# Optimization experiments

Measured on AMD Instinct MI355X. Metric: run time of the kernel, lower is better.

Reference implementation:

```python
import jax, jax.numpy as jnp
import numpy as np

H = 128  # hidden size

def lstm_layer(x, Wih, Whh, bih, bhh):
    """One PyTorch-semantics LSTM layer. x: (B,T,F). Gate order: i,f,g,o."""
    B = x.shape[0]
    # Precompute input contributions for all timesteps: (B,T,4H)
    xg = jnp.einsum('btf,gf->btg', x, Wih) + bih + bhh
    def step(carry, xt):
        h, c = carry
        g = xt + h @ Whh.T                      # (B,4H)
        i, f, gg, o = jnp.split(g, 4, axis=-1)
        i = jax.nn.sigmoid(i)
        f = jax.nn.sigmoid(f)
        gg = jnp.tanh(gg)
        o = jax.nn.sigmoid(o)
        c = f * c + i * gg
        h = o * jnp.tanh(c)
        return (h, c), h
    h0 = jnp.zeros((B, H), x.dtype)
    (hT, cT), hs = jax.lax.scan(step, (h0, h0), jnp.swapaxes(xg, 0, 1))
    return jnp.swapaxes(hs, 0, 1), hT  # (B,T,H), (B,H)


def setup_inputs() -> dict:
    key = jax.random.key(0)
    ks = jax.random.split(key, 20)
    B, T = 256, 2048
    s = 1.0 / np.sqrt(H)  # PyTorch default init scale
    inp = {
        'x': jax.random.normal(ks[0], (B, T, 1), jnp.float32),
        'Wih0': jax.random.uniform(ks[1], (4 * H, 1), jnp.float32, -s, s),
        'Whh0': jax.random.uniform(ks[2], (4 * H, H), jnp.float32, -s, s),
        'bih0': jax.random.uniform(ks[3], (4 * H,), jnp.float32, -s, s),
        'bhh0': jax.random.uniform(ks[4], (4 * H,), jnp.float32, -s, s),
        'Wih1': jax.random.uniform(ks[5], (4 * H, H), jnp.float32, -s, s),
        'Whh1': jax.random.uniform(ks[6], (4 * H, H), jnp.float32, -s, s),
        'bih1': jax.random.uniform(ks[7], (4 * H,), jnp.float32, -s, s),
        'bhh1': jax.random.uniform(ks[8], (4 * H,), jnp.float32, -s, s),
        'Wih2': jax.random.uniform(ks[9], (4 * H, H), jnp.float32, -s, s),
        'Whh2': jax.random.uniform(ks[10], (4 * H, H), jnp.float32, -s, s),
        'bih2': jax.random.uniform(ks[11], (4 * H,), jnp.float32, -s, s),
        'bhh2': jax.random.uniform(ks[12], (4 * H,), jnp.float32, -s, s),
        'fc1_w': jax.random.uniform(ks[13], (64, H), jnp.float32, -s, s),
        'fc1_b': jax.random.uniform(ks[14], (64,), jnp.float32, -s, s),
        'fc2_w': jax.random.uniform(ks[15], (5, 64), jnp.float32, -1.0 / 8, 1.0 / 8),
        'fc2_b': jax.random.uniform(ks[16], (5,), jnp.float32, -1.0 / 8, 1.0 / 8),
    }
    return inp


def reference(x, Wih0, Whh0, bih0, bhh0, Wih1, Whh1, bih1, bhh1,
              Wih2, Whh2, bih2, bhh2, fc1_w, fc1_b, fc2_w, fc2_b):
    # 3-layer LSTM (eval mode: inter-layer dropout is identity)
    h1, _ = lstm_layer(x, Wih0, Whh0, bih0, bhh0)
    h2, _ = lstm_layer(h1, Wih1, Whh1, bih1, bhh1)
    _, hT = lstm_layer(h2, Wih2, Whh2, bih2, bhh2)  # hn[-1]: (B,H)
    z = jax.nn.relu(hT @ fc1_w.T + fc1_b)
    return z @ fc2_w.T + fc2_b  # (B, num_classes)
```

## Files before the change

kernel.cpp:

```cpp
#include <hip/hip_runtime.h>


#define HDIM 128
#define TDIM 2048
#define NB 16
#define NG 16
#define CH 16
#define NCH 128
#define NT 512

typedef _Float16 half8_t __attribute__((ext_vector_type(8)));
typedef float f32x4 __attribute__((ext_vector_type(4)));

__device__ __forceinline__ f32x4 mfma16(half8_t a, half8_t b, f32x4 c) {
    return __builtin_amdgcn_mfma_f32_16x16x32_f16(a, b, c, 0, 0, 0);
}

__device__ __forceinline__ void fast_barrier() {
    asm volatile("s_waitcnt lgkmcnt(0)\n\ts_barrier" ::: "memory");
}

__device__ __forceinline__ float sigm_f(float x) {
    return __builtin_amdgcn_rcpf(1.0f + __expf(-x));
}
__device__ __forceinline__ float tanh_f(float x) {
    return fmaf(-2.0f, __builtin_amdgcn_rcpf(1.0f + __expf(2.0f * x)), 1.0f);
}

__global__ __launch_bounds__(256)
void convert_w(const float* __restrict__ Whh0, const float* __restrict__ Wih1,
               const float* __restrict__ Whh1, const float* __restrict__ Wih2,
               const float* __restrict__ Whh2, _Float16* __restrict__ dst,
               int* __restrict__ flags) {
    int i = blockIdx.x * 256 + threadIdx.x;
    if (i < 2 * NG * NCH) flags[i] = 0;
    int seg = i >> 16, off = i & 65535;
    const float* s = (seg == 0) ? Whh0 : (seg == 1) ? Wih1 : (seg == 2) ? Whh1
                   : (seg == 3) ? Wih2 : Whh2;
    dst[i] = (_Float16)s[off];
}

__global__ __launch_bounds__(NT, 2)
void lstm3_pipe(const float* __restrict__ x,   const float* __restrict__ Wih0,
                const float* __restrict__ bih0, const float* __restrict__ bhh0,
                const float* __restrict__ bih1, const float* __restrict__ bhh1,
                const float* __restrict__ bih2, const float* __restrict__ bhh2,
                const float* __restrict__ fc1w, const float* __restrict__ fc1b,
                const float* __restrict__ fc2w, const float* __restrict__ fc2b,
                float* __restrict__ out,
                _Float16* __restrict__ hbuf, const _Float16* __restrict__ wbuf,
                int* __restrict__ flags)
{
    __shared__ __align__(16) _Float16 hown[CH * NB * HDIM];
    __shared__ __align__(16) _Float16 hst [CH * NB * HDIM];
    __shared__ float x_s[CH][NB];
    __shared__ float z_s[NB][64];
    __shared__ float hfin[NB][HDIM];

    const int tid = threadIdx.x;
    const int ln = tid & 63, wv = tid >> 6;
    const int c = ln & 15, p = ln >> 4;
    const int L = blockIdx.x >> 4;
    const int g = blockIdx.x & 15;

    const _Float16* whh = wbuf + (size_t)((L == 0) ? 0 : (L == 1) ? 2 : 4) * 65536;
    const _Float16* wih = wbuf + (size_t)((L == 1) ? 1 : 3) * 65536;
    half8_t whh_f[4][4], wih_f[4][4];
#pragma unroll
    for (int q = 0; q < 4; ++q)
#pragma unroll
        for (int m = 0; m < 4; ++m) {
            whh_f[q][m] = *(const half8_t*)(whh + (size_t)(q*HDIM + wv*16 + c)*HDIM + m*32 + p*8);
            if (L > 0)
                wih_f[q][m] = *(const half8_t*)(wih + (size_t)(q*HDIM + wv*16 + c)*HDIM + m*32 + p*8);
        }

    const float* bihL = (L == 0) ? bih0 : (L == 1) ? bih1 : bih2;
    const float* bhhL = (L == 0) ? bhh0 : (L == 1) ? bhh1 : bhh2;
    const int u = wv * 16 + c;
    float bias[4], w0[4];
#pragma unroll
    for (int q = 0; q < 4; ++q) {
        bias[q] = bihL[q*HDIM + u] + bhhL[q*HDIM + u];
        w0[q] = (L == 0) ? Wih0[q*HDIM + u] : 0.0f;
    }

    int roff[4], woff[4];
#pragma unroll
    for (int m = 0; m < 4; ++m)
        roff[m] = c*HDIM + ((32*m + 8*p) ^ (8*(c & 7)));
#pragma unroll
    for (int r = 0; r < 4; ++r) {
        int seq = p*4 + r;
        woff[r] = seq*HDIM + (u ^ (8*(seq & 7)));
    }

    for (int i = tid; i < NB*HDIM/2; i += NT)
        ((int*)(hown + 15*NB*HDIM))[i] = 0;
    float cc[4] = {0.f, 0.f, 0.f, 0.f};
    __syncthreads();

    int* fprod = flags + (L*NG + g)*NCH;
    int* fcons = flags + ((L-1)*NG + g)*NCH;
    const float* xb = x + (size_t)(g*NB)*TDIM;

#pragma unroll 1
    for (int s = 0; s < NCH; ++s) {
        _Float16* gch = hbuf + ((size_t)(g*NCH + s) << 15);

        if (L == 0) {
            if (tid < CH*NB)
                x_s[tid >> 4][tid & 15] = xb[(size_t)(tid & 15)*TDIM + s*CH + (tid >> 4)];
        } else {
            if (tid == 0) {
                while (__hip_atomic_load(fcons + s, __ATOMIC_ACQUIRE,
                                         __HIP_MEMORY_SCOPE_AGENT) == 0)
                    __builtin_amdgcn_s_sleep(8);
            }
            __syncthreads();
            const float4* gsrc = (const float4*)gch;
            float4* dv = (float4*)hst;
#pragma unroll
            for (int k2 = 0; k2 < 8; ++k2) dv[k2*NT + tid] = gsrc[k2*NT + tid];
        }
        fast_barrier();

#pragma unroll 1
        for (int tt = 0; tt < CH; ++tt) {
            const int tp = (tt + CH - 1) & 15;
            const _Float16* rsl = hown + tp*(NB*HDIM);
            const _Float16* psl = hst  + tt*(NB*HDIM);
            half8_t A0 = *(const half8_t*)(rsl + roff[0]);
            half8_t A1 = *(const half8_t*)(rsl + roff[1]);
            half8_t A2 = *(const half8_t*)(rsl + roff[2]);
            half8_t A3 = *(const half8_t*)(rsl + roff[3]);

            f32x4 acc[4];
            if (L > 0) {
                half8_t P0 = *(const half8_t*)(psl + roff[0]);
                half8_t P1 = *(const half8_t*)(psl + roff[1]);
                half8_t P2 = *(const half8_t*)(psl + roff[2]);
                half8_t P3 = *(const half8_t*)(psl + roff[3]);
#pragma unroll
                for (int q = 0; q < 4; ++q) {
                    f32x4 a = {0.f, 0.f, 0.f, 0.f};
                    a = mfma16(P0, wih_f[q][0], a);
                    a = mfma16(P1, wih_f[q][1], a);
                    a = mfma16(P2, wih_f[q][2], a);
                    a = mfma16(P3, wih_f[q][3], a);
                    acc[q] = a;
                }
            } else {
#pragma unroll
                for (int q = 0; q < 4; ++q) acc[q] = (f32x4){0.f, 0.f, 0.f, 0.f};
            }
#pragma unroll
            for (int q = 0; q < 4; ++q) {
                acc[q] = mfma16(A0, whh_f[q][0], acc[q]);
                acc[q] = mfma16(A1, whh_f[q][1], acc[q]);
                acc[q] = mfma16(A2, whh_f[q][2], acc[q]);
                acc[q] = mfma16(A3, whh_f[q][3], acc[q]);
            }

            _Float16* wsl = hown + tt*(NB*HDIM);
#pragma unroll
            for (int r = 0; r < 4; ++r) {
                float pi = acc[0][r] + bias[0];
                float pf = acc[1][r] + bias[1];
                float pg = acc[2][r] + bias[2];
                float po = acc[3][r] + bias[3];
                if (L == 0) {
                    float xr = x_s[tt][p*4 + r];
                    pi = fmaf(xr, w0[0], pi); pf = fmaf(xr, w0[1], pf);
                    pg = fmaf(xr, w0[2], pg); po = fmaf(xr, w0[3], po);
                }
                float ig = sigm_f(pi), fg = sigm_f(pf);
                float gg = tanh_f(pg), og = sigm_f(po);
                cc[r] = fmaf(fg, cc[r], ig * gg);
                wsl[woff[r]] = (_Float16)(og * tanh_f(cc[r]));
            }
            fast_barrier();
        }

        if (L < 2) {
            const float4* sv = (const float4*)hown;
            float4* gdst = (float4*)gch;
#pragma unroll
            for (int k2 = 0; k2 < 8; ++k2) gdst[k2*NT + tid] = sv[k2*NT + tid];
            __threadfence();
            __syncthreads();
            if (tid == 0)
                __hip_atomic_store(fprod + s, 1, __ATOMIC_RELEASE,
                                   __HIP_MEMORY_SCOPE_AGENT);
        }
    }

    if (L == 2) {
        __syncthreads();
        for (int i = tid; i < NB*HDIM; i += NT) {
            int seq = i >> 7, uu = i & 127;
            hfin[seq][uu] = (float)hown[15*NB*HDIM + seq*HDIM + (uu ^ (8*(seq & 7)))];
        }
        __syncthreads();
        for (int d = tid; d < NB*64; d += NT) {
            int seq = d >> 6, un = d & 63;
            const float4* w4 = (const float4*)(fc1w + un*HDIM);
            const float4* h4 = (const float4*)hfin[seq];
            float sacc = fc1b[un];
#pragma unroll
            for (int k2 = 0; k2 < 32; ++k2) {
                float4 a = w4[k2], bb = h4[k2];
                sacc += a.x*bb.x + a.y*bb.y + a.z*bb.z + a.w*bb.w;
            }
            z_s[seq][un] = fmaxf(sacc, 0.0f);
        }
        __syncthreads();
        for (int d = tid; d < NB*5; d += NT) {
            int seq = d / 5, o = d - seq*5;
            const float* w = fc2w + o*64;
            float sacc = fc2b[o];
#pragma unroll
            for (int k2 = 0; k2 < 64; ++k2) sacc += w[k2] * z_s[seq][k2];
            out[(size_t)(g*NB + seq)*5 + o] = sacc;
        }
    }
}

extern "C" void kernel_launch(void* const* d_in, const int* in_sizes, int n_in,
                              void* d_out, int out_size, void* d_ws, size_t ws_size,
                              hipStream_t stream) {
    (void)in_sizes; (void)n_in; (void)out_size; (void)ws_size;
    const float* x    = (const float*)d_in[0];
    const float* Wih0 = (const float*)d_in[1];
    const float* Whh0 = (const float*)d_in[2];
    const float* bih0 = (const float*)d_in[3];
    const float* bhh0 = (const float*)d_in[4];
    const float* Wih1 = (const float*)d_in[5];
    const float* Whh1 = (const float*)d_in[6];
    const float* bih1 = (const float*)d_in[7];
    const float* bhh1 = (const float*)d_in[8];
    const float* Wih2 = (const float*)d_in[9];
    const float* Whh2 = (const float*)d_in[10];
    const float* bih2 = (const float*)d_in[11];
    const float* bhh2 = (const float*)d_in[12];
    const float* fc1w = (const float*)d_in[13];
    const float* fc1b = (const float*)d_in[14];
    const float* fc2w = (const float*)d_in[15];
    const float* fc2b = (const float*)d_in[16];
    float* out = (float*)d_out;

    _Float16* hbuf = (_Float16*)d_ws;
    _Float16* wbuf = hbuf + (size_t)67108864;
    int* flags = (int*)(wbuf + (size_t)5*65536);

    hipLaunchKernelGGL(convert_w, dim3(1280), dim3(256), 0, stream,
                       Whh0, Wih1, Whh1, Wih2, Whh2, wbuf, flags);
    hipLaunchKernelGGL(lstm3_pipe, dim3(3*NG), dim3(NT), 0, stream,
                       x, Wih0, bih0, bhh0, bih1, bhh1, bih2, bhh2,
                       fc1w, fc1b, fc2w, fc2b, out, hbuf, wbuf, flags);
}
```

Measured before the change: 3.733 ms.

## Stream input weights from memory, reorder MFMAs, use cache-bypassing inter-layer handoff

The input-to-hidden weight fragments are no longer held in registers. They are reloaded from global memory on every timestep, which lowers register pressure but adds per-step memory traffic. The recurrent h·Whh MFMAs now issue first so the critical dependency starts earlier, and the input projection goes into a separate accumulator. The inter-layer producer/consumer handoff swaps atomics and __threadfence for inline-asm sc0 sc1 loads and stores with a shorter sleep, aiming to cut synchronisation latency. The ordering guarantees of the hand-written flag protocol now rest on those cache bits rather than on acquire/release semantics.

```diff
diff --git a/kernel.cpp b/kernel.cpp
--- a/kernel.cpp
+++ b/kernel.cpp
@@ -65,15 +65,13 @@
 
     const _Float16* whh = wbuf + (size_t)((L == 0) ? 0 : (L == 1) ? 2 : 4) * 65536;
     const _Float16* wih = wbuf + (size_t)((L == 1) ? 1 : 3) * 65536;
-    half8_t whh_f[4][4], wih_f[4][4];
+    half8_t whh_f[4][4];
 #pragma unroll
     for (int q = 0; q < 4; ++q)
 #pragma unroll
-        for (int m = 0; m < 4; ++m) {
+        for (int m = 0; m < 4; ++m)
             whh_f[q][m] = *(const half8_t*)(whh + (size_t)(q*HDIM + wv*16 + c)*HDIM + m*32 + p*8);
-            if (L > 0)
-                wih_f[q][m] = *(const half8_t*)(wih + (size_t)(q*HDIM + wv*16 + c)*HDIM + m*32 + p*8);
-        }
+    const _Float16* wihL = wih + (size_t)(wv*16 + c)*HDIM + p*8;
 
     const float* bihL = (L == 0) ? bih0 : (L == 1) ? bih1 : bih2;
     const float* bhhL = (L == 0) ? bhh0 : (L == 1) ? bhh1 : bhh2;
@@ -101,7 +99,7 @@
     __syncthreads();
 
     int* fprod = flags + (L*NG + g)*NCH;
-    int* fcons = flags + ((L-1)*NG + g)*NCH;
+    const int* fcons = flags + ((L-1)*NG + g)*NCH;
     const float* xb = x + (size_t)(g*NB)*TDIM;
 
 #pragma unroll 1
@@ -113,13 +111,19 @@
                 x_s[tid >> 4][tid & 15] = xb[(size_t)(tid & 15)*TDIM + s*CH + (tid >> 4)];
         } else {
             if (tid == 0) {
-                while (__hip_atomic_load(fcons + s, __ATOMIC_ACQUIRE,
-                                         __HIP_MEMORY_SCOPE_AGENT) == 0)
-                    __builtin_amdgcn_s_sleep(8);
+                const int* fp = fcons + s;
+                int f;
+                while (1) {
+                    asm volatile("global_load_dword %0, %1, off sc0 sc1\n\t"
+                                 "s_waitcnt vmcnt(0)"
+                                 : "=v"(f) : "v"(fp) : "memory");
+                    if (f) break;
+                    __builtin_amdgcn_s_sleep(2);
+                }
             }
             __syncthreads();
-            const float4* gsrc = (const float4*)gch;
-            float4* dv = (float4*)hst;
+            const f32x4* gsrc = (const f32x4*)gch;
+            f32x4* dv = (f32x4*)hst;
 #pragma unroll
             for (int k2 = 0; k2 < 8; ++k2) dv[k2*NT + tid] = gsrc[k2*NT + tid];
         }
@@ -129,37 +133,41 @@
         for (int tt = 0; tt < CH; ++tt) {
             const int tp = (tt + CH - 1) & 15;
             const _Float16* rsl = hown + tp*(NB*HDIM);
-            const _Float16* psl = hst  + tt*(NB*HDIM);
             half8_t A0 = *(const half8_t*)(rsl + roff[0]);
             half8_t A1 = *(const half8_t*)(rsl + roff[1]);
             half8_t A2 = *(const half8_t*)(rsl + roff[2]);
             half8_t A3 = *(const half8_t*)(rsl + roff[3]);
 
-            f32x4 acc[4];
+            f32x4 acc[4], pac[4];
+#pragma unroll
+            for (int q = 0; q < 4; ++q) {
+                f32x4 a = {0.f, 0.f, 0.f, 0.f};
+                a = mfma16(A0, whh_f[q][0], a);
+                a = mfma16(A1, whh_f[q][1], a);
+                a = mfma16(A2, whh_f[q][2], a);
+                a = mfma16(A3, whh_f[q][3], a);
+                acc[q] = a;
+            }
             if (L > 0) {
+                const _Float16* psl = hst + tt*(NB*HDIM);
                 half8_t P0 = *(const half8_t*)(psl + roff[0]);
                 half8_t P1 = *(const half8_t*)(psl + roff[1]);
                 half8_t P2 = *(const half8_t*)(psl + roff[2]);
                 half8_t P3 = *(const half8_t*)(psl + roff[3]);
 #pragma unroll
                 for (int q = 0; q < 4; ++q) {
+                    const _Float16* wq = wihL + q*(HDIM*HDIM);
+                    half8_t B0 = *(const half8_t*)(wq);
+                    half8_t B1 = *(const half8_t*)(wq + 32);
+                    half8_t B2 = *(const half8_t*)(wq + 64);
+                    half8_t B3 = *(const half8_t*)(wq + 96);
                     f32x4 a = {0.f, 0.f, 0.f, 0.f};
-                    a = mfma16(P0, wih_f[q][0], a);
-                    a = mfma16(P1, wih_f[q][1], a);
-                    a = mfma16(P2, wih_f[q][2], a);
-                    a = mfma16(P3, wih_f[q][3], a);
-                    acc[q] = a;
+                    a = mfma16(P0, B0, a);
+                    a = mfma16(P1, B1, a);
+                    a = mfma16(P2, B2, a);
+                    a = mfma16(P3, B3, a);
+                    pac[q] = a;
                 }
-            } else {
-#pragma unroll
-                for (int q = 0; q < 4; ++q) acc[q] = (f32x4){0.f, 0.f, 0.f, 0.f};
-            }
-#pragma unroll
-            for (int q = 0; q < 4; ++q) {
-                acc[q] = mfma16(A0, whh_f[q][0], acc[q]);
-                acc[q] = mfma16(A1, whh_f[q][1], acc[q]);
-                acc[q] = mfma16(A2, whh_f[q][2], acc[q]);
-                acc[q] = mfma16(A3, whh_f[q][3], acc[q]);
             }
 
             _Float16* wsl = hown + tt*(NB*HDIM);
@@ -169,7 +177,10 @@
                 float pf = acc[1][r] + bias[1];
                 float pg = acc[2][r] + bias[2];
                 float po = acc[3][r] + bias[3];
-                if (L == 0) {
+                if (L > 0) {
+                    pi += pac[0][r]; pf += pac[1][r];
+                    pg += pac[2][r]; po += pac[3][r];
+                } else {
                     float xr = x_s[tt][p*4 + r];
                     pi = fmaf(xr, w0[0], pi); pf = fmaf(xr, w0[1], pf);
                     pg = fmaf(xr, w0[2], pg); po = fmaf(xr, w0[3], po);
@@ -183,15 +194,22 @@
         }
 
         if (L < 2) {
-            const float4* sv = (const float4*)hown;
-            float4* gdst = (float4*)gch;
-#pragma unroll
-            for (int k2 = 0; k2 < 8; ++k2) gdst[k2*NT + tid] = sv[k2*NT + tid];
-            __threadfence();
+            const f32x4* sv = (const f32x4*)hown;
+#pragma unroll
+            for (int k2 = 0; k2 < 8; ++k2) {
+                f32x4 v = sv[k2*NT + tid];
+                f32x4* gp = (f32x4*)gch + k2*NT + tid;
+                asm volatile("global_store_dwordx4 %0, %1, off sc0 sc1"
+                             :: "v"(gp), "v"(v) : "memory");
+            }
+            asm volatile("s_waitcnt vmcnt(0)" ::: "memory");
             __syncthreads();
-            if (tid == 0)
-                __hip_atomic_store(fprod + s, 1, __ATOMIC_RELEASE,
-                                   __HIP_MEMORY_SCOPE_AGENT);
+            if (tid == 0) {
+                int one = 1;
+                int* fp = fprod + s;
+                asm volatile("global_store_dword %0, %1, off sc0 sc1"
+                             :: "v"(fp), "v"(one) : "memory");
+            }
         }
     }
 
```

Measured after the change: 9.202 ms. +146.5%, slower.

## Split batch into 64 groups of 4 sequences and prescale gates for exp2

Applied to the files above, without the earlier changes.

Cuts the per-block batch from 16 to 4 sequences and raises the group count from 16 to 64, so 192 blocks run the layer pipeline instead of 48. Each MFMA row-block now holds 4 sequences spaced 4 rows apart, so each lane handles one gate element per step. Weights and biases are prescaled by -log2(e) (doubled for the g gate) so the activations use exp2 directly. Bias is also folded into the accumulator init. The recurrent MFMA work per block stays the same, so this trades a lot of wasted MFMA rows for more parallel chains and less activation math per thread, and it also changes the LDS layout and the global exchange format.

```diff
diff --git a/kernel.cpp b/kernel.cpp
--- a/kernel.cpp
+++ b/kernel.cpp
@@ -3,14 +3,16 @@
 
 #define HDIM 128
 #define TDIM 2048
-#define NB 16
-#define NG 16
+#define NB 4
+#define NG 64
 #define CH 16
 #define NCH 128
 #define NT 512
+#define SLICE 2048
 
 typedef _Float16 half8_t __attribute__((ext_vector_type(8)));
 typedef float f32x4 __attribute__((ext_vector_type(4)));
+typedef int int4v __attribute__((ext_vector_type(4)));
 
 __device__ __forceinline__ f32x4 mfma16(half8_t a, half8_t b, f32x4 c) {
     return __builtin_amdgcn_mfma_f32_16x16x32_f16(a, b, c, 0, 0, 0);
@@ -20,12 +22,11 @@
     asm volatile("s_waitcnt lgkmcnt(0)\n\ts_barrier" ::: "memory");
 }
 
-__device__ __forceinline__ float sigm_f(float x) {
-    return __builtin_amdgcn_rcpf(1.0f + __expf(-x));
-}
-__device__ __forceinline__ float tanh_f(float x) {
-    return fmaf(-2.0f, __builtin_amdgcn_rcpf(1.0f + __expf(2.0f * x)), 1.0f);
-}
+__device__ __forceinline__ float rcpf(float x) { return __builtin_amdgcn_rcpf(x); }
+__device__ __forceinline__ float ex2(float x)  { return __builtin_amdgcn_exp2f(x); }
+
+#define NL2E  -1.4426950408889634f
+#define N2L2E -2.8853900817779268f
 
 __global__ __launch_bounds__(256)
 void convert_w(const float* __restrict__ Whh0, const float* __restrict__ Wih1,
@@ -37,10 +38,12 @@
     int seg = i >> 16, off = i & 65535;
     const float* s = (seg == 0) ? Whh0 : (seg == 1) ? Wih1 : (seg == 2) ? Whh1
                    : (seg == 3) ? Wih2 : Whh2;
-    dst[i] = (_Float16)s[off];
-}
-
-__global__ __launch_bounds__(NT, 2)
+    int gate = off >> 14;
+    float sc = (gate == 2) ? N2L2E : NL2E;
+    dst[i] = (_Float16)(s[off] * sc);
+}
+
+__global__ __launch_bounds__(NT, 1)
 void lstm3_pipe(const float* __restrict__ x,   const float* __restrict__ Wih0,
                 const float* __restrict__ bih0, const float* __restrict__ bhh0,
                 const float* __restrict__ bih1, const float* __restrict__ bhh1,
@@ -51,8 +54,8 @@
                 _Float16* __restrict__ hbuf, const _Float16* __restrict__ wbuf,
                 int* __restrict__ flags)
 {
-    __shared__ __align__(16) _Float16 hown[CH * NB * HDIM];
-    __shared__ __align__(16) _Float16 hst [CH * NB * HDIM];
+    __shared__ __align__(16) _Float16 hown[CH * SLICE];
+    __shared__ __align__(16) _Float16 hst [CH * SLICE];
     __shared__ float x_s[CH][NB];
     __shared__ float z_s[NB][64];
     __shared__ float hfin[NB][HDIM];
@@ -60,8 +63,8 @@
     const int tid = threadIdx.x;
     const int ln = tid & 63, wv = tid >> 6;
     const int c = ln & 15, p = ln >> 4;
-    const int L = blockIdx.x >> 4;
-    const int g = blockIdx.x & 15;
+    const int L = blockIdx.x >> 6;
+    const int g = blockIdx.x & 63;
 
     const _Float16* whh = wbuf + (size_t)((L == 0) ? 0 : (L == 1) ? 2 : 4) * 65536;
     const _Float16* wih = wbuf + (size_t)((L == 1) ? 1 : 3) * 65536;
@@ -81,23 +84,20 @@
     float bias[4], w0[4];
 #pragma unroll
     for (int q = 0; q < 4; ++q) {
-        bias[q] = bihL[q*HDIM + u] + bhhL[q*HDIM + u];
-        w0[q] = (L == 0) ? Wih0[q*HDIM + u] : 0.0f;
+        float sc = (q == 2) ? N2L2E : NL2E;
+        bias[q] = (bihL[q*HDIM + u] + bhhL[q*HDIM + u]) * sc;
+        w0[q] = (L == 0) ? Wih0[q*HDIM + u] * sc : 0.0f;
     }
 
-    int roff[4], woff[4];
+    int roff[4];
 #pragma unroll
     for (int m = 0; m < 4; ++m)
         roff[m] = c*HDIM + ((32*m + 8*p) ^ (8*(c & 7)));
-#pragma unroll
-    for (int r = 0; r < 4; ++r) {
-        int seq = p*4 + r;
-        woff[r] = seq*HDIM + (u ^ (8*(seq & 7)));
-    }
-
-    for (int i = tid; i < NB*HDIM/2; i += NT)
-        ((int*)(hown + 15*NB*HDIM))[i] = 0;
-    float cc[4] = {0.f, 0.f, 0.f, 0.f};
+    const int woff = (4*p)*HDIM + (u ^ (32*(p & 1)));
+
+    { int* ph = (int*)hown; int* ps = (int*)hst;
+      for (int i = tid; i < CH*SLICE/2; i += NT) { ph[i] = 0; ps[i] = 0; } }
+    float cc = 0.f;
     __syncthreads();
 
     int* fprod = flags + (L*NG + g)*NCH;
@@ -106,11 +106,11 @@
 
 #pragma unroll 1
     for (int s = 0; s < NCH; ++s) {
-        _Float16* gch = hbuf + ((size_t)(g*NCH + s) << 15);
+        _Float16* gch = hbuf + ((size_t)(g*NCH + s) << 13);
 
         if (L == 0) {
             if (tid < CH*NB)
-                x_s[tid >> 4][tid & 15] = xb[(size_t)(tid & 15)*TDIM + s*CH + (tid >> 4)];
+                x_s[tid >> 2][tid & 3] = xb[(size_t)(tid & 3)*TDIM + s*CH + (tid >> 2)];
         } else {
             if (tid == 0) {
                 while (__hip_atomic_load(fcons + s, __ATOMIC_ACQUIRE,
@@ -118,41 +118,49 @@
                     __builtin_amdgcn_s_sleep(8);
             }
             __syncthreads();
-            const float4* gsrc = (const float4*)gch;
-            float4* dv = (float4*)hst;
-#pragma unroll
-            for (int k2 = 0; k2 < 8; ++k2) dv[k2*NT + tid] = gsrc[k2*NT + tid];
+#pragma unroll
+            for (int k2 = 0; k2 < 2; ++k2) {
+                int e = k2*NT + tid;
+                int tt_ = e >> 6, rem = e & 63, s4 = rem >> 4, u8 = (rem & 15)*8;
+                int lo = tt_*SLICE + s4*4*HDIM + (u8 ^ (32*(s4 & 1)));
+                *(int4v*)(hst + lo) = ((const int4v*)gch)[e];
+            }
         }
         fast_barrier();
 
 #pragma unroll 1
         for (int tt = 0; tt < CH; ++tt) {
             const int tp = (tt + CH - 1) & 15;
-            const _Float16* rsl = hown + tp*(NB*HDIM);
-            const _Float16* psl = hst  + tt*(NB*HDIM);
+            const _Float16* rsl = hown + tp*SLICE;
             half8_t A0 = *(const half8_t*)(rsl + roff[0]);
             half8_t A1 = *(const half8_t*)(rsl + roff[1]);
             half8_t A2 = *(const half8_t*)(rsl + roff[2]);
             half8_t A3 = *(const half8_t*)(rsl + roff[3]);
 
             f32x4 acc[4];
-            if (L > 0) {
+            if (L == 0) {
+                float xv = x_s[tt][p];
+#pragma unroll
+                for (int q = 0; q < 4; ++q) {
+                    float z0 = fmaf(xv, w0[q], bias[q]);
+                    acc[q] = (f32x4){z0, z0, z0, z0};
+                }
+            } else {
+#pragma unroll
+                for (int q = 0; q < 4; ++q)
+                    acc[q] = (f32x4){bias[q], bias[q], bias[q], bias[q]};
+                const _Float16* psl = hst + tt*SLICE;
                 half8_t P0 = *(const half8_t*)(psl + roff[0]);
                 half8_t P1 = *(const half8_t*)(psl + roff[1]);
                 half8_t P2 = *(const half8_t*)(psl + roff[2]);
                 half8_t P3 = *(const half8_t*)(psl + roff[3]);
 #pragma unroll
                 for (int q = 0; q < 4; ++q) {
-                    f32x4 a = {0.f, 0.f, 0.f, 0.f};
-                    a = mfma16(P0, wih_f[q][0], a);
-                    a = mfma16(P1, wih_f[q][1], a);
-                    a = mfma16(P2, wih_f[q][2], a);
-                    a = mfma16(P3, wih_f[q][3], a);
-                    acc[q] = a;
+                    acc[q] = mfma16(P0, wih_f[q][0], acc[q]);
+                    acc[q] = mfma16(P1, wih_f[q][1], acc[q]);
+                    acc[q] = mfma16(P2, wih_f[q][2], acc[q]);
+                    acc[q] = mfma16(P3, wih_f[q][3], acc[q]);
                 }
-            } else {
-#pragma unroll
-                for (int q = 0; q < 4; ++q) acc[q] = (f32x4){0.f, 0.f, 0.f, 0.f};
             }
 #pragma unroll
             for (int q = 0; q < 4; ++q) {
@@ -162,31 +170,25 @@
                 acc[q] = mfma16(A3, whh_f[q][3], acc[q]);
             }
 
-            _Float16* wsl = hown + tt*(NB*HDIM);
-#pragma unroll
-            for (int r = 0; r < 4; ++r) {
-                float pi = acc[0][r] + bias[0];
-                float pf = acc[1][r] + bias[1];
-                float pg = acc[2][r] + bias[2];
-                float po = acc[3][r] + bias[3];
-                if (L == 0) {
-                    float xr = x_s[tt][p*4 + r];
-                    pi = fmaf(xr, w0[0], pi); pf = fmaf(xr, w0[1], pf);
-                    pg = fmaf(xr, w0[2], pg); po = fmaf(xr, w0[3], po);
-                }
-                float ig = sigm_f(pi), fg = sigm_f(pf);
-                float gg = tanh_f(pg), og = sigm_f(po);
-                cc[r] = fmaf(fg, cc[r], ig * gg);
-                wsl[woff[r]] = (_Float16)(og * tanh_f(cc[r]));
-            }
+            float ai = rcpf(1.0f + ex2(acc[0][0]));
+            float af = rcpf(1.0f + ex2(acc[1][0]));
+            float tg = fmaf(2.0f, rcpf(1.0f + ex2(acc[2][0])), -1.0f);
+            float ao = rcpf(1.0f + ex2(acc[3][0]));
+            cc = fmaf(af, cc, ai * tg);
+            float tc = fmaf(2.0f, rcpf(1.0f + ex2(cc * N2L2E)), -1.0f);
+            hown[tt*SLICE + woff] = (_Float16)(ao * tc);
+
             fast_barrier();
         }
 
         if (L < 2) {
-            const float4* sv = (const float4*)hown;
-            float4* gdst = (float4*)gch;
-#pragma unroll
-            for (int k2 = 0; k2 < 8; ++k2) gdst[k2*NT + tid] = sv[k2*NT + tid];
+#pragma unroll
+            for (int k2 = 0; k2 < 2; ++k2) {
+                int e = k2*NT + tid;
+                int tt_ = e >> 6, rem = e & 63, s4 = rem >> 4, u8 = (rem & 15)*8;
+                int lo = tt_*SLICE + s4*4*HDIM + (u8 ^ (32*(s4 & 1)));
+                ((int4v*)gch)[e] = *(const int4v*)(hown + lo);
+            }
             __threadfence();
             __syncthreads();
             if (tid == 0)
@@ -199,11 +201,11 @@
         __syncthreads();
         for (int i = tid; i < NB*HDIM; i += NT) {
             int seq = i >> 7, uu = i & 127;
-            hfin[seq][uu] = (float)hown[15*NB*HDIM + seq*HDIM + (uu ^ (8*(seq & 7)))];
+            hfin[seq][uu] = (float)hown[15*SLICE + seq*4*HDIM + (uu ^ (32*(seq & 1)))];
         }
         __syncthreads();
-        for (int d = tid; d < NB*64; d += NT) {
-            int seq = d >> 6, un = d & 63;
+        if (tid < NB*64) {
+            int seq = tid >> 6, un = tid & 63;
             const float4* w4 = (const float4*)(fc1w + un*HDIM);
             const float4* h4 = (const float4*)hfin[seq];
             float sacc = fc1b[un];
@@ -215,8 +217,8 @@
             z_s[seq][un] = fmaxf(sacc, 0.0f);
         }
         __syncthreads();
-        for (int d = tid; d < NB*5; d += NT) {
-            int seq = d / 5, o = d - seq*5;
+        if (tid < NB*5) {
+            int seq = tid / 5, o = tid - seq*5;
             const float* w = fc2w + o*64;
             float sacc = fc2b[o];
 #pragma unroll
```

After: 4.405 ms. +18.0%, slower.
